# Kernel optimization log

Measured on AMD Instinct MI355X. Metric: run time of the kernel, lower is better.

## Reference

```python
import jax, jax.numpy as jnp
import numpy as np

B, T, H, D = 4, 4096, 16, 64
BLOCK_SIZE = 64      # BS: local block size
NUM_GLOBAL = 64      # G: global tokens (first G positions)
NUM_RANDOM = 192     # R: random key positions shared by all blocks


def setup_inputs() -> dict:
    key = jax.random.key(0)
    kq, kk, kv, kr = jax.random.split(key, 4)
    q = jax.random.normal(kq, (B, T, H, D), dtype=jnp.float32)
    k = jax.random.normal(kk, (B, T, H, D), dtype=jnp.float32)
    v = jax.random.normal(kv, (B, T, H, D), dtype=jnp.float32)
    # torch.randperm(src_len)[:R] -> no duplicate indices
    rand_idx = jax.random.permutation(kr, T)[:NUM_RANDOM].astype(jnp.int32)
    return {"q": q, "k": k, "v": v, "rand_idx": rand_idx}


def _bigbird(q, k, v, rand_idx):
    Bq, Tq, Hq, Dq = q.shape
    inv_scale = Dq ** (-0.5)
    G, BS, R = NUM_GLOBAL, BLOCK_SIZE, NUM_RANDOM

    # --- global queries: full attention over all keys ---
    gs = jnp.einsum('bghd,bkhd->bhgk', q[:, :G], k) * inv_scale
    gw = jax.nn.softmax(gs, axis=-1)
    out_g = jnp.einsum('bhgk,bkhd->bghd', gw, v)  # (B, G, H, D)

    # --- non-global queries: local block + global + random keys, one softmax ---
    nb = (Tq - G) // BS  # (T - G) divisible by BS by construction
    qb = q[:, G:].reshape(Bq, nb, BS, Hq, Dq)
    kb = k[:, G:].reshape(Bq, nb, BS, Hq, Dq)
    vb = v[:, G:].reshape(Bq, nb, BS, Hq, Dq)
    kg, vg = k[:, :G], v[:, :G]            # (B, G, H, D)
    kr, vr = k[:, rand_idx], v[:, rand_idx]  # (B, R, H, D)

    s_loc = jnp.einsum('bnlhd,bnkhd->bnhlk', qb, kb)   # (B, nb, H, BS, BS)
    s_glo = jnp.einsum('bnlhd,bkhd->bnhlk', qb, kg)    # (B, nb, H, BS, G)
    s_rnd = jnp.einsum('bnlhd,bkhd->bnhlk', qb, kr)    # (B, nb, H, BS, R)
    s = jnp.concatenate([s_loc, s_glo, s_rnd], axis=-1) * inv_scale
    w = jax.nn.softmax(s, axis=-1)  # joint softmax over local|global|random keys
    w_loc, w_glo, w_rnd = w[..., :BS], w[..., BS:BS + G], w[..., BS + G:]

    out_b = (jnp.einsum('bnhlk,bnkhd->bnlhd', w_loc, vb)
             + jnp.einsum('bnhlk,bkhd->bnlhd', w_glo, vg)
             + jnp.einsum('bnhlk,bkhd->bnlhd', w_rnd, vr))
    out_b = out_b.reshape(Bq, Tq - G, Hq, Dq)

    return jnp.concatenate([out_g, out_b], axis=1)  # (B, T, H, D)


def reference(q, k, v, rand_idx):
    return _bigbird(q, k, v, rand_idx)
```

## Files before the change

kernel.cpp:

```cpp
#include <hip/hip_runtime.h>
#include <math.h>
#include <stdint.h>

#define BB 4
#define TT 4096
#define HH 16
#define DD 64
#define GG 64
#define NRND 192
#define HD 1024
#define NBH 64
#define NCHUNK 4
#define NGBLK (NBH*NCHUNK)
#define NSPB  (NBH*63)

#define OFF_KBF  0ull
#define OFF_VT   33554432ull
#define OFF_KRT  67108864ull
#define OFF_VRT  68681728ull
#define OFF_WACC 70254592ull
#define OFF_WM   74448896ull
#define OFF_WL   74514432ull

typedef __attribute__((ext_vector_type(8))) short short8;
typedef __attribute__((ext_vector_type(16))) float f32x16;

__device__ __forceinline__ ushort rne_u(float f) {
    uint32_t u = __builtin_bit_cast(uint32_t, f);
    u += 0x7fffu + ((u >> 16) & 1u);
    return (ushort)(u >> 16);
}
__device__ __forceinline__ short bf_trunc_s(float f) {
    uint32_t u = __builtin_bit_cast(uint32_t, f);
    return (short)(u >> 16);
}
__device__ __forceinline__ float bf_back(short s) {
    uint32_t u = ((uint32_t)(uint16_t)s) << 16;
    return __builtin_bit_cast(float, u);
}
__device__ __forceinline__ short8 ld8u(const ushort* p) {
    typedef __attribute__((ext_vector_type(4))) short short4v;
    short4v a = *(const short4v*)p;
    short4v b = *(const short4v*)(p + 4);
    short8 r;
    r[0]=a[0]; r[1]=a[1]; r[2]=a[2]; r[3]=a[3];
    r[4]=b[0]; r[5]=b[1]; r[6]=b[2]; r[7]=b[3];
    return r;
}

typedef const __attribute__((address_space(1))) uint32_t* gas1_t;
typedef __attribute__((address_space(3))) uint32_t* las3_t;
__device__ __forceinline__ void gld16(const void* g, void* l) {
    __builtin_amdgcn_global_load_lds((gas1_t)g, (las3_t)l, 16, 0, 0);
}

__global__ __launch_bounds__(256, 4)
void bb_prep(const float* __restrict__ K, const float* __restrict__ V,
             const int* __restrict__ RIDX, char* __restrict__ ws)
{
    __shared__ ushort tl[64][68];
    __shared__ int toks[NRND];
    const int bid = blockIdx.x, tid = threadIdx.x;
    const int r  = tid >> 2;
    const int d0 = (tid & 3) * 16;

    if (bid < 8192) {
        const bool isK = bid < 4096;
        const int id = isK ? bid : bid - 4096;
        const int bh = id >> 6, tile = id & 63;
        const int b = bh >> 4, h = bh & 15;
        const float* src = (isK ? K : V) + ((size_t)b*TT*HH + h)*DD
                         + (size_t)(tile*64 + r)*HD + d0;
        float f[16];
        #pragma unroll
        for (int i = 0; i < 16; i += 4) {
            const float4 v4 = *(const float4*)(src + i);
            f[i]=v4.x; f[i+1]=v4.y; f[i+2]=v4.z; f[i+3]=v4.w;
        }
        if (isK) {
            #pragma unroll
            for (int i = 0; i < 16; ++i) tl[r][d0+i] = rne_u(f[i]);
        } else {
            #pragma unroll
            for (int i = 0; i < 16; ++i) tl[d0+i][r] = rne_u(f[i]);
        }
        __syncthreads();
        char* obase = ws + (isK ? OFF_KBF : OFF_VT)
                    + (size_t)bh*524288 + (size_t)tile*8192;
        #pragma unroll
        for (int e = 0; e < 2; ++e) {
            const int uu = tid*2 + e;
            const int c = uu >> 6, rr = uu & 63;
            *(short8*)(obase + c*1024 + rr*16) = ld8u(&tl[rr][c*8]);
        }
    } else {
        const int bh = bid - 8192;
        const int b = bh >> 4, h = bh & 15;
        const size_t base = ((size_t)b*TT*HH + h)*DD;
        if (tid < NRND) toks[tid] = RIDX[tid];
        __syncthreads();
        for (int sub = 0; sub < 3; ++sub) {
            const int tok = toks[sub*64 + r];
            float f[16];
            const float* ks = K + base + (size_t)tok*HD + d0;
            #pragma unroll
            for (int i = 0; i < 16; i += 4) {
                const float4 v4 = *(const float4*)(ks + i);
                f[i]=v4.x; f[i+1]=v4.y; f[i+2]=v4.z; f[i+3]=v4.w;
            }
            #pragma unroll
            for (int i = 0; i < 16; ++i) tl[r][d0+i] = rne_u(f[i]);
            __syncthreads();
            {
                char* obase = ws + OFF_KRT + (size_t)bh*24576 + (size_t)sub*8192;
                #pragma unroll
                for (int e = 0; e < 2; ++e) {
                    const int uu = tid*2 + e;
                    const int c = uu >> 6, rr = uu & 63;
                    *(short8*)(obase + c*1024 + rr*16) = ld8u(&tl[rr][c*8]);
                }
            }
            __syncthreads();
            const float* vs = V + base + (size_t)tok*HD + d0;
            #pragma unroll
            for (int i = 0; i < 16; i += 4) {
                const float4 v4 = *(const float4*)(vs + i);
                f[i]=v4.x; f[i+1]=v4.y; f[i+2]=v4.z; f[i+3]=v4.w;
            }
            #pragma unroll
            for (int i = 0; i < 16; ++i) tl[d0+i][r] = rne_u(f[i]);
            __syncthreads();
            {
                char* obase = ws + OFF_VRT + (size_t)bh*24576 + (size_t)sub*8192;
                #pragma unroll
                for (int e = 0; e < 2; ++e) {
                    const int uu = tid*2 + e;
                    const int c = uu >> 6, rr = uu & 63;
                    *(short8*)(obase + c*1024 + rr*16) = ld8u(&tl[rr][c*8]);
                }
            }
            __syncthreads();
        }
    }
}

__global__ __launch_bounds__(256, 4)
void bb_mfma(const float* __restrict__ Q, float* __restrict__ OUT,
             char* __restrict__ ws)
{
    __shared__ __align__(16) char smem[32768];
    __shared__ float sm_m[2][64];
    __shared__ float sm_l[2][64];
    float (*osum)[67] = (float(*)[67])smem;

    const int tid  = threadIdx.x;
    const int lane = tid & 63;
    const int wid  = tid >> 6;
    const int wq   = wid >> 1;
    const int wk   = wid & 1;
    const int lq   = lane & 31;
    const int lh   = lane >> 5;

    const int j = blockIdx.x;
    const bool is_glob = j < NGBLK;
    int bh, qtok0, ntiles, kt0 = 0, chunk = 0;
    if (is_glob) {
        chunk = j >> 6;
        bh    = (j & 7) + 8 * ((j >> 3) & 7);
        kt0   = chunk * 16;
        qtok0 = 0; ntiles = 16;
    } else {
        const int js = j - NGBLK;
        bh    = (js & 7) + 8 * ((js >> 3) & 7);
        qtok0 = GG + (js >> 6) * 64;
        ntiles = 5;
    }
    const int b  = bh >> 4;
    const int hd = bh & 15;
    const size_t bh_off = ((size_t)b * TT * HH + hd) * DD;

    const char* kbf_bh = ws + OFF_KBF + (size_t)bh * 524288;
    const char* vt_bh  = ws + OFF_VT  + (size_t)bh * 524288;
    const char* krt_bh = ws + OFF_KRT + (size_t)bh * 24576;
    const char* vrt_bh = ws + OFF_VRT + (size_t)bh * 24576;

    auto kbase = [&](int kt) -> const char* {
        if (is_glob)     return kbf_bh + (size_t)(kt0 + kt) * 8192;
        if (kt == 0)     return kbf_bh + (size_t)(qtok0 >> 6) * 8192;
        if (kt == 1)     return kbf_bh;
        return krt_bh + (size_t)(kt - 2) * 8192;
    };
    auto vbase = [&](int kt) -> const char* {
        if (is_glob)     return vt_bh + (size_t)(kt0 + kt) * 8192;
        if (kt == 0)     return vt_bh + (size_t)(qtok0 >> 6) * 8192;
        if (kt == 1)     return vt_bh;
        return vrt_bh + (size_t)(kt - 2) * 8192;
    };

    float4 qa[4], qb[4];
    {
        const float* qp = Q + bh_off + (size_t)(qtok0 + wq*32 + lq) * HD;
        #pragma unroll
        for (int ks = 0; ks < 4; ++ks) {
            qa[ks] = *(const float4*)(qp + ks*16 + lh*8);
            qb[ks] = *(const float4*)(qp + ks*16 + lh*8 + 4);
        }
    }

    auto stage = [&](int buf, int kt_t) {
        const char* kb = kbase(kt_t);
        const char* vb = vbase(kt_t);
        #pragma unroll
        for (int i = 0; i < 2; ++i) {
            const int c = wid*2 + i;
            gld16(kb + c*1024 + lane*16, smem + buf*8192 + c*1024);
            gld16(vb + c*1024 + lane*16, smem + 16384 + buf*8192 + c*1024);
        }
    };
    stage(0, 0);

    const float QSC = 0.18033688f;
    short8 qfh[4], qfl[4];
    #pragma unroll
    for (int ks = 0; ks < 4; ++ks) {
        float fv[8] = {qa[ks].x, qa[ks].y, qa[ks].z, qa[ks].w,
                       qb[ks].x, qb[ks].y, qb[ks].z, qb[ks].w};
        #pragma unroll
        for (int jj = 0; jj < 8; ++jj) {
            const float x = fv[jj] * QSC;
            const short hi = bf_trunc_s(x);
            qfh[ks][jj] = hi;
            qfl[ks][jj] = bf_trunc_s(x - bf_back(hi));
        }
    }

    f32x16 acc0, acc1;
    #pragma unroll
    for (int r = 0; r < 16; ++r) { acc0[r] = 0.f; acc1[r] = 0.f; }
    float m_run = -INFINITY, l_run = 0.f;

    for (int kt = 0; kt < ntiles; ++kt) {
        const int cur = kt & 1;
        const bool hn = (kt + 1 < ntiles);
        if (hn) {
            stage(cur ^ 1, kt + 1);
            asm volatile("s_waitcnt vmcnt(4)" ::: "memory");
        } else {
            asm volatile("s_waitcnt vmcnt(0)" ::: "memory");
        }
        __builtin_amdgcn_s_barrier();
        asm volatile("" ::: "memory");

        const char* kb = smem + cur*8192;
        const char* vb = smem + 16384 + cur*8192;

        f32x16 sc;
        #pragma unroll
        for (int r = 0; r < 16; ++r) sc[r] = 0.f;
        {
            const int krow = wk*32 + lq;
            #pragma unroll
            for (int ks = 0; ks < 4; ++ks) {
                const short8 ak = *(const short8*)(kb + (ks*2 + lh)*1024 + krow*16);
                sc = __builtin_amdgcn_mfma_f32_32x32x16_bf16(ak, qfh[ks], sc, 0, 0, 0);
                sc = __builtin_amdgcn_mfma_f32_32x32x16_bf16(ak, qfl[ks], sc, 0, 0, 0);
            }
        }

        float pm = sc[0];
        #pragma unroll
        for (int r = 1; r < 16; ++r) pm = fmaxf(pm, sc[r]);
        pm = fmaxf(pm, __shfl_xor(pm, 32));
        if (__any(pm > m_run + 11.5f)) {
            const float mnew = fmaxf(m_run, pm);
            const float cf = __builtin_exp2f(m_run - mnew);
            l_run *= cf;
            #pragma unroll
            for (int r = 0; r < 16; ++r) { acc0[r] *= cf; acc1[r] *= cf; }
            m_run = mnew;
        }
        float ls = 0.f;
        #pragma unroll
        for (int r = 0; r < 16; ++r) {
            sc[r] = __builtin_exp2f(sc[r] - m_run);
            ls += sc[r];
        }
        ls += __shfl_xor(ls, 32);
        l_run += ls;

        #pragma unroll
        for (int s = 0; s < 2; ++s) {
            uint32_t a01, a23, a45, a67;
            asm("v_cvt_pk_bf16_f32 %0, %1, %2" : "=v"(a01) : "v"(sc[8*s+0]), "v"(sc[8*s+1]));
            asm("v_cvt_pk_bf16_f32 %0, %1, %2" : "=v"(a23) : "v"(sc[8*s+2]), "v"(sc[8*s+3]));
            asm("v_cvt_pk_bf16_f32 %0, %1, %2" : "=v"(a45) : "v"(sc[8*s+4]), "v"(sc[8*s+5]));
            asm("v_cvt_pk_bf16_f32 %0, %1, %2" : "=v"(a67) : "v"(sc[8*s+6]), "v"(sc[8*s+7]));
            asm("v_permlane32_swap_b32 %0, %1" : "+v"(a01), "+v"(a45));
            asm("v_permlane32_swap_b32 %0, %1" : "+v"(a23), "+v"(a67));
            union { uint32_t u[4]; short8 v; } pfu;
            pfu.u[0] = a01; pfu.u[1] = a23; pfu.u[2] = a45; pfu.u[3] = a67;
            const int cb = wk*4 + s*2 + lh;
            const short8 v0 = *(const short8*)(vb + cb*1024 + lq*16);
            const short8 v1 = *(const short8*)(vb + cb*1024 + (lq + 32)*16);
            acc0 = __builtin_amdgcn_mfma_f32_32x32x16_bf16(v0, pfu.v, acc0, 0, 0, 0);
            acc1 = __builtin_amdgcn_mfma_f32_32x32x16_bf16(v1, pfu.v, acc1, 0, 0, 0);
        }

        if (hn) {
            asm volatile("" ::: "memory");
            __builtin_amdgcn_s_barrier();
            asm volatile("" ::: "memory");
        }
    }

    if (lane < 32) { sm_m[wk][wq*32 + lq] = m_run; sm_l[wk][wq*32 + lq] = l_run; }
    __syncthreads();
    const int qrow = wq*32 + lq;
    const float Mq  = fmaxf(sm_m[0][qrow], sm_m[1][qrow]);
    const float wsc = __builtin_exp2f(m_run - Mq);
    if (wk == 0) {
        #pragma unroll
        for (int r = 0; r < 16; ++r) {
            const int dr = (r & 3) + 8*(r >> 2) + 4*lh;
            osum[qrow][dr     ] = acc0[r] * wsc;
            osum[qrow][dr + 32] = acc1[r] * wsc;
        }
    }
    __syncthreads();
    if (wk == 1) {
        #pragma unroll
        for (int r = 0; r < 16; ++r) {
            const int dr = (r & 3) + 8*(r >> 2) + 4*lh;
            osum[qrow][dr     ] += acc0[r] * wsc;
            osum[qrow][dr + 32] += acc1[r] * wsc;
        }
    }
    __syncthreads();
    {
        const int q  = tid >> 2;
        const int d0 = (tid & 3) * 16;
        const float M     = fmaxf(sm_m[0][q], sm_m[1][q]);
        const float lcomb = __builtin_exp2f(sm_m[0][q] - M) * sm_l[0][q]
                          + __builtin_exp2f(sm_m[1][q] - M) * sm_l[1][q];
        if (is_glob) {
            float* WACC = (float*)(ws + OFF_WACC);
            float* WM   = (float*)(ws + OFF_WM);
            float* WL   = (float*)(ws + OFF_WL);
            const int slot = chunk * NBH + bh;
            float* dst = WACC + (size_t)slot * 4096 + q * 64 + d0;
            #pragma unroll
            for (int i = 0; i < 16; i += 4) {
                float4 o;
                o.x = osum[q][d0 + i    ];
                o.y = osum[q][d0 + i + 1];
                o.z = osum[q][d0 + i + 2];
                o.w = osum[q][d0 + i + 3];
                *(float4*)(dst + i) = o;
            }
            if ((tid & 3) == 0) {
                WM[slot * 64 + q] = M;
                WL[slot * 64 + q] = lcomb;
            }
        } else {
            const float inv = 1.f / lcomb;
            float* dst = OUT + bh_off + (size_t)(qtok0 + q) * HD + d0;
            #pragma unroll
            for (int i = 0; i < 16; i += 4) {
                float4 o;
                o.x = osum[q][d0 + i    ] * inv;
                o.y = osum[q][d0 + i + 1] * inv;
                o.z = osum[q][d0 + i + 2] * inv;
                o.w = osum[q][d0 + i + 3] * inv;
                *(float4*)(dst + i) = o;
            }
        }
    }
}

__global__ __launch_bounds__(256, 4)
void bb_combine(const char* __restrict__ ws, float* __restrict__ OUT)
{
    const int bh = blockIdx.x;
    const int b  = bh >> 4;
    const int hd = bh & 15;
    const size_t bh_off = ((size_t)b * TT * HH + hd) * DD;

    const float* WACC = (const float*)(ws + OFF_WACC);
    const float* WM   = (const float*)(ws + OFF_WM);
    const float* WL   = (const float*)(ws + OFF_WL);

    const int q  = threadIdx.x >> 2;
    const int d0 = (threadIdx.x & 3) * 16;

    float m[NCHUNK];
    float M = -INFINITY;
    #pragma unroll
    for (int c = 0; c < NCHUNK; ++c) {
        m[c] = WM[(c * NBH + bh) * 64 + q];
        M = fmaxf(M, m[c]);
    }
    float w[NCHUNK];
    float denom = 0.f;
    #pragma unroll
    for (int c = 0; c < NCHUNK; ++c) {
        w[c] = __builtin_exp2f(m[c] - M);
        denom += w[c] * WL[(c * NBH + bh) * 64 + q];
    }
    const float inv = 1.f / denom;

    float* dst = OUT + bh_off + (size_t)q * HD + d0;
    #pragma unroll
    for (int i = 0; i < 16; i += 4) {
        float ox = 0.f, oy = 0.f, oz = 0.f, ow = 0.f;
        #pragma unroll
        for (int c = 0; c < NCHUNK; ++c) {
            const float4 a = *(const float4*)&WACC[(size_t)(c * NBH + bh) * 4096 + q * 64 + d0 + i];
            ox += w[c] * a.x; oy += w[c] * a.y;
            oz += w[c] * a.z; ow += w[c] * a.w;
        }
        float4 o; o.x = ox * inv; o.y = oy * inv; o.z = oz * inv; o.w = ow * inv;
        *(float4*)(dst + i) = o;
    }
}

extern "C" void kernel_launch(void* const* d_in, const int* in_sizes, int n_in,
                              void* d_out, int out_size, void* d_ws, size_t ws_size,
                              hipStream_t stream) {
    const float* Q    = (const float*)d_in[0];
    const float* K    = (const float*)d_in[1];
    const float* V    = (const float*)d_in[2];
    const int*   RIDX = (const int*)d_in[3];
    float* OUT = (float*)d_out;
    char*  ws  = (char*)d_ws;

    hipLaunchKernelGGL(bb_prep, dim3(8192 + 64), dim3(256), 0, stream,
                       K, V, RIDX, ws);
    hipLaunchKernelGGL(bb_mfma, dim3(NGBLK + NSPB), dim3(256), 0, stream,
                       Q, OUT, ws);
    hipLaunchKernelGGL(bb_combine, dim3(NBH), dim3(256), 0, stream, ws, OUT);
}
```

Measured before the change: 123.1 us.

## Process 128-query blocks per workgroup to share global/random K/V tiles

Result: slower. 132.3 us (+7.5%).

```diff
diff --git a/kernel.cpp b/kernel.cpp
--- a/kernel.cpp
+++ b/kernel.cpp
@@ -10,9 +10,10 @@
 #define NRND 192
 #define HD 1024
 #define NBH 64
+#define QBLK 128
+#define NSPQ 32
 #define NCHUNK 4
-#define NGBLK (NBH*NCHUNK)
-#define NSPB  (NBH*63)
+#define SUBS (NCHUNK + NSPQ)
 
 #define OFF_KBF  0ull
 #define OFF_VT   33554432ull
@@ -37,6 +38,13 @@
 __device__ __forceinline__ float bf_back(short s) {
     uint32_t u = ((uint32_t)(uint16_t)s) << 16;
     return __builtin_bit_cast(float, u);
+}
+__device__ __forceinline__ float exp2_fast(float x) {
+#if __has_builtin(__builtin_amdgcn_exp2f)
+    return __builtin_amdgcn_exp2f(x);
+#else
+    float r; asm("v_exp_f32 %0, %1" : "=v"(r) : "v"(x)); return r;
+#endif
 }
 __device__ __forceinline__ short8 ld8u(const ushort* p) {
     typedef __attribute__((ext_vector_type(4))) short short4v;
@@ -144,13 +152,13 @@
     }
 }
 
-__global__ __launch_bounds__(256, 4)
+__global__ __launch_bounds__(512, 4)
 void bb_mfma(const float* __restrict__ Q, float* __restrict__ OUT,
              char* __restrict__ ws)
 {
-    __shared__ __align__(16) char smem[32768];
-    __shared__ float sm_m[2][64];
-    __shared__ float sm_l[2][64];
+    __shared__ __align__(16) char smem[34816];
+    __shared__ float sm_m[2][QBLK];
+    __shared__ float sm_l[2][QBLK];
     float (*osum)[67] = (float(*)[67])smem;
 
     const int tid  = threadIdx.x;
@@ -162,18 +170,19 @@
     const int lh   = lane >> 5;
 
     const int j = blockIdx.x;
-    const bool is_glob = j < NGBLK;
-    int bh, qtok0, ntiles, kt0 = 0, chunk = 0;
+    const int r = j & 63;
+    const int bh = ((r & 7) << 3) | (r >> 3);
+    const int sub = j >> 6;
+    const bool is_glob = sub < NCHUNK;
+    int qtok0, ntiles, kt0 = 0, chunk = 0, tA = 0, tB = 0;
     if (is_glob) {
-        chunk = j >> 6;
-        bh    = (j & 7) + 8 * ((j >> 3) & 7);
-        kt0   = chunk * 16;
-        qtok0 = 0; ntiles = 16;
+        chunk = sub; kt0 = chunk * 16; qtok0 = 0; ntiles = 16;
     } else {
-        const int js = j - NGBLK;
-        bh    = (js & 7) + 8 * ((js >> 3) & 7);
-        qtok0 = GG + (js >> 6) * 64;
-        ntiles = 5;
+        const int qi = sub - NCHUNK;
+        qtok0 = GG + qi * QBLK;
+        tA = 1 + 2 * qi;
+        tB = (qi == 31) ? 63 : 2 + 2 * qi;
+        ntiles = 6;
     }
     const int b  = bh >> 4;
     const int hd = bh & 15;
@@ -185,21 +194,27 @@
     const char* vrt_bh = ws + OFF_VRT + (size_t)bh * 24576;
 
     auto kbase = [&](int kt) -> const char* {
-        if (is_glob)     return kbf_bh + (size_t)(kt0 + kt) * 8192;
-        if (kt == 0)     return kbf_bh + (size_t)(qtok0 >> 6) * 8192;
-        if (kt == 1)     return kbf_bh;
-        return krt_bh + (size_t)(kt - 2) * 8192;
+        if (is_glob) return kbf_bh + (size_t)(kt0 + kt) * 8192;
+        if (kt == 0) return kbf_bh + (size_t)tA * 8192;
+        if (kt == 1) return kbf_bh + (size_t)tB * 8192;
+        if (kt == 2) return kbf_bh;
+        return krt_bh + (size_t)(kt - 3) * 8192;
     };
     auto vbase = [&](int kt) -> const char* {
-        if (is_glob)     return vt_bh + (size_t)(kt0 + kt) * 8192;
-        if (kt == 0)     return vt_bh + (size_t)(qtok0 >> 6) * 8192;
-        if (kt == 1)     return vt_bh;
-        return vrt_bh + (size_t)(kt - 2) * 8192;
+        if (is_glob) return vt_bh + (size_t)(kt0 + kt) * 8192;
+        if (kt == 0) return vt_bh + (size_t)tA * 8192;
+        if (kt == 1) return vt_bh + (size_t)tB * 8192;
+        if (kt == 2) return vt_bh;
+        return vrt_bh + (size_t)(kt - 3) * 8192;
     };
 
+    const int qrow = wq * 32 + lq;
+    int qoff;
+    if (is_glob) qoff = qrow & 63;
+    else         qoff = (qtok0 + qrow < TT) ? qrow : (qrow & 63);
     float4 qa[4], qb[4];
     {
-        const float* qp = Q + bh_off + (size_t)(qtok0 + wq*32 + lq) * HD;
+        const float* qp = Q + bh_off + (size_t)(qtok0 + qoff) * HD;
         #pragma unroll
         for (int ks = 0; ks < 4; ++ks) {
             qa[ks] = *(const float4*)(qp + ks*16 + lh*8);
@@ -207,15 +222,13 @@
         }
     }
 
+    char* kbuf = smem;
+    char* vbuf = smem + 16384;
     auto stage = [&](int buf, int kt_t) {
         const char* kb = kbase(kt_t);
         const char* vb = vbase(kt_t);
-        #pragma unroll
-        for (int i = 0; i < 2; ++i) {
-            const int c = wid*2 + i;
-            gld16(kb + c*1024 + lane*16, smem + buf*8192 + c*1024);
-            gld16(vb + c*1024 + lane*16, smem + 16384 + buf*8192 + c*1024);
-        }
+        gld16(kb + wid*1024 + lane*16, kbuf + buf*8192 + wid*1024);
+        gld16(vb + wid*1024 + lane*16, vbuf + buf*8192 + wid*1024);
     };
     stage(0, 0);
 
@@ -236,7 +249,7 @@
 
     f32x16 acc0, acc1;
     #pragma unroll
-    for (int r = 0; r < 16; ++r) { acc0[r] = 0.f; acc1[r] = 0.f; }
+    for (int rr = 0; rr < 16; ++rr) { acc0[rr] = 0.f; acc1[rr] = 0.f; }
     float m_run = -INFINITY, l_run = 0.f;
 
     for (int kt = 0; kt < ntiles; ++kt) {
@@ -244,66 +257,75 @@
         const bool hn = (kt + 1 < ntiles);
         if (hn) {
             stage(cur ^ 1, kt + 1);
-            asm volatile("s_waitcnt vmcnt(4)" ::: "memory");
+            asm volatile("s_waitcnt vmcnt(2)" ::: "memory");
         } else {
             asm volatile("s_waitcnt vmcnt(0)" ::: "memory");
         }
         __builtin_amdgcn_s_barrier();
         asm volatile("" ::: "memory");
 
-        const char* kb = smem + cur*8192;
-        const char* vb = smem + 16384 + cur*8192;
-
-        f32x16 sc;
-        #pragma unroll
-        for (int r = 0; r < 16; ++r) sc[r] = 0.f;
-        {
-            const int krow = wk*32 + lq;
-            #pragma unroll
-            for (int ks = 0; ks < 4; ++ks) {
-                const short8 ak = *(const short8*)(kb + (ks*2 + lh)*1024 + krow*16);
-                sc = __builtin_amdgcn_mfma_f32_32x32x16_bf16(ak, qfh[ks], sc, 0, 0, 0);
-                sc = __builtin_amdgcn_mfma_f32_32x32x16_bf16(ak, qfl[ks], sc, 0, 0, 0);
-            }
-        }
-
-        float pm = sc[0];
-        #pragma unroll
-        for (int r = 1; r < 16; ++r) pm = fmaxf(pm, sc[r]);
-        pm = fmaxf(pm, __shfl_xor(pm, 32));
-        if (__any(pm > m_run + 11.5f)) {
-            const float mnew = fmaxf(m_run, pm);
-            const float cf = __builtin_exp2f(m_run - mnew);
-            l_run *= cf;
-            #pragma unroll
-            for (int r = 0; r < 16; ++r) { acc0[r] *= cf; acc1[r] *= cf; }
-            m_run = mnew;
-        }
-        float ls = 0.f;
-        #pragma unroll
-        for (int r = 0; r < 16; ++r) {
-            sc[r] = __builtin_exp2f(sc[r] - m_run);
-            ls += sc[r];
-        }
-        ls += __shfl_xor(ls, 32);
-        l_run += ls;
-
-        #pragma unroll
-        for (int s = 0; s < 2; ++s) {
-            uint32_t a01, a23, a45, a67;
-            asm("v_cvt_pk_bf16_f32 %0, %1, %2" : "=v"(a01) : "v"(sc[8*s+0]), "v"(sc[8*s+1]));
-            asm("v_cvt_pk_bf16_f32 %0, %1, %2" : "=v"(a23) : "v"(sc[8*s+2]), "v"(sc[8*s+3]));
-            asm("v_cvt_pk_bf16_f32 %0, %1, %2" : "=v"(a45) : "v"(sc[8*s+4]), "v"(sc[8*s+5]));
-            asm("v_cvt_pk_bf16_f32 %0, %1, %2" : "=v"(a67) : "v"(sc[8*s+6]), "v"(sc[8*s+7]));
-            asm("v_permlane32_swap_b32 %0, %1" : "+v"(a01), "+v"(a45));
-            asm("v_permlane32_swap_b32 %0, %1" : "+v"(a23), "+v"(a67));
-            union { uint32_t u[4]; short8 v; } pfu;
-            pfu.u[0] = a01; pfu.u[1] = a23; pfu.u[2] = a45; pfu.u[3] = a67;
-            const int cb = wk*4 + s*2 + lh;
-            const short8 v0 = *(const short8*)(vb + cb*1024 + lq*16);
-            const short8 v1 = *(const short8*)(vb + cb*1024 + (lq + 32)*16);
-            acc0 = __builtin_amdgcn_mfma_f32_32x32x16_bf16(v0, pfu.v, acc0, 0, 0, 0);
-            acc1 = __builtin_amdgcn_mfma_f32_32x32x16_bf16(v1, pfu.v, acc1, 0, 0, 0);
+        const bool act = is_glob ? true
+                       : (kt == 0) ? (wq < 2)
+                       : (kt == 1) ? (wq >= 2) : true;
+        if (act) {
+            const char* kb = kbuf + cur*8192;
+            const char* vb = vbuf + cur*8192;
+
+            f32x16 sc;
+            #pragma unroll
+            for (int rr = 0; rr < 16; ++rr) sc[rr] = 0.f;
+            {
+                const int krow = wk*32 + lq;
+                __builtin_amdgcn_s_setprio(1);
+                #pragma unroll
+                for (int ks = 0; ks < 4; ++ks) {
+                    const short8 ak = *(const short8*)(kb + (ks*2 + lh)*1024 + krow*16);
+                    sc = __builtin_amdgcn_mfma_f32_32x32x16_bf16(ak, qfh[ks], sc, 0, 0, 0);
+                    sc = __builtin_amdgcn_mfma_f32_32x32x16_bf16(ak, qfl[ks], sc, 0, 0, 0);
+                }
+                __builtin_amdgcn_s_setprio(0);
+            }
+
+            float pm = sc[0];
+            #pragma unroll
+            for (int rr = 1; rr < 16; ++rr) pm = fmaxf(pm, sc[rr]);
+            pm = fmaxf(pm, __shfl_xor(pm, 32));
+            if (__any(pm > m_run + 11.5f)) {
+                const float mnew = fmaxf(m_run, pm);
+                const float cf = exp2_fast(m_run - mnew);
+                l_run *= cf;
+                #pragma unroll
+                for (int rr = 0; rr < 16; ++rr) { acc0[rr] *= cf; acc1[rr] *= cf; }
+                m_run = mnew;
+            }
+            float ls = 0.f;
+            #pragma unroll
+            for (int rr = 0; rr < 16; ++rr) {
+                sc[rr] = exp2_fast(sc[rr] - m_run);
+                ls += sc[rr];
+            }
+            ls += __shfl_xor(ls, 32);
+            l_run += ls;
+
+            #pragma unroll
+            for (int s = 0; s < 2; ++s) {
+                uint32_t a01, a23, a45, a67;
+                asm("v_cvt_pk_bf16_f32 %0, %1, %2" : "=v"(a01) : "v"(sc[8*s+0]), "v"(sc[8*s+1]));
+                asm("v_cvt_pk_bf16_f32 %0, %1, %2" : "=v"(a23) : "v"(sc[8*s+2]), "v"(sc[8*s+3]));
+                asm("v_cvt_pk_bf16_f32 %0, %1, %2" : "=v"(a45) : "v"(sc[8*s+4]), "v"(sc[8*s+5]));
+                asm("v_cvt_pk_bf16_f32 %0, %1, %2" : "=v"(a67) : "v"(sc[8*s+6]), "v"(sc[8*s+7]));
+                asm("v_permlane32_swap_b32 %0, %1" : "+v"(a01), "+v"(a45));
+                asm("v_permlane32_swap_b32 %0, %1" : "+v"(a23), "+v"(a67));
+                union { uint32_t u[4]; short8 v; } pfu;
+                pfu.u[0] = a01; pfu.u[1] = a23; pfu.u[2] = a45; pfu.u[3] = a67;
+                const int cb = wk*4 + s*2 + lh;
+                const short8 v0 = *(const short8*)(vb + cb*1024 + lq*16);
+                const short8 v1 = *(const short8*)(vb + cb*1024 + (lq + 32)*16);
+                __builtin_amdgcn_s_setprio(1);
+                acc0 = __builtin_amdgcn_mfma_f32_32x32x16_bf16(v0, pfu.v, acc0, 0, 0, 0);
+                acc1 = __builtin_amdgcn_mfma_f32_32x32x16_bf16(v1, pfu.v, acc1, 0, 0, 0);
+                __builtin_amdgcn_s_setprio(0);
+            }
         }
 
         if (hn) {
@@ -313,26 +335,25 @@
         }
     }
 
-    if (lane < 32) { sm_m[wk][wq*32 + lq] = m_run; sm_l[wk][wq*32 + lq] = l_run; }
+    if (lane < 32) { sm_m[wk][qrow] = m_run; sm_l[wk][qrow] = l_run; }
     __syncthreads();
-    const int qrow = wq*32 + lq;
     const float Mq  = fmaxf(sm_m[0][qrow], sm_m[1][qrow]);
-    const float wsc = __builtin_exp2f(m_run - Mq);
+    const float wsc = exp2_fast(m_run - Mq);
     if (wk == 0) {
         #pragma unroll
-        for (int r = 0; r < 16; ++r) {
-            const int dr = (r & 3) + 8*(r >> 2) + 4*lh;
-            osum[qrow][dr     ] = acc0[r] * wsc;
-            osum[qrow][dr + 32] = acc1[r] * wsc;
+        for (int rr = 0; rr < 16; ++rr) {
+            const int dr = (rr & 3) + 8*(rr >> 2) + 4*lh;
+            osum[qrow][dr     ] = acc0[rr] * wsc;
+            osum[qrow][dr + 32] = acc1[rr] * wsc;
         }
     }
     __syncthreads();
     if (wk == 1) {
         #pragma unroll
-        for (int r = 0; r < 16; ++r) {
-            const int dr = (r & 3) + 8*(r >> 2) + 4*lh;
-            osum[qrow][dr     ] += acc0[r] * wsc;
-            osum[qrow][dr + 32] += acc1[r] * wsc;
+        for (int rr = 0; rr < 16; ++rr) {
+            const int dr = (rr & 3) + 8*(rr >> 2) + 4*lh;
+            osum[qrow][dr     ] += acc0[rr] * wsc;
+            osum[qrow][dr + 32] += acc1[rr] * wsc;
         }
     }
     __syncthreads();
@@ -340,28 +361,30 @@
         const int q  = tid >> 2;
         const int d0 = (tid & 3) * 16;
         const float M     = fmaxf(sm_m[0][q], sm_m[1][q]);
-        const float lcomb = __builtin_exp2f(sm_m[0][q] - M) * sm_l[0][q]
-                          + __builtin_exp2f(sm_m[1][q] - M) * sm_l[1][q];
+        const float lcomb = exp2_fast(sm_m[0][q] - M) * sm_l[0][q]
+                          + exp2_fast(sm_m[1][q] - M) * sm_l[1][q];
         if (is_glob) {
-            float* WACC = (float*)(ws + OFF_WACC);
-            float* WM   = (float*)(ws + OFF_WM);
-            float* WL   = (float*)(ws + OFF_WL);
-            const int slot = chunk * NBH + bh;
-            float* dst = WACC + (size_t)slot * 4096 + q * 64 + d0;
-            #pragma unroll
-            for (int i = 0; i < 16; i += 4) {
-                float4 o;
-                o.x = osum[q][d0 + i    ];
-                o.y = osum[q][d0 + i + 1];
-                o.z = osum[q][d0 + i + 2];
-                o.w = osum[q][d0 + i + 3];
-                *(float4*)(dst + i) = o;
-            }
-            if ((tid & 3) == 0) {
-                WM[slot * 64 + q] = M;
-                WL[slot * 64 + q] = lcomb;
-            }
-        } else {
+            if (q < 64) {
+                float* WACC = (float*)(ws + OFF_WACC);
+                float* WM   = (float*)(ws + OFF_WM);
+                float* WL   = (float*)(ws + OFF_WL);
+                const int slot = chunk * NBH + bh;
+                float* dst = WACC + (size_t)slot * 4096 + q * 64 + d0;
+                #pragma unroll
+                for (int i = 0; i < 16; i += 4) {
+                    float4 o;
+                    o.x = osum[q][d0 + i    ];
+                    o.y = osum[q][d0 + i + 1];
+                    o.z = osum[q][d0 + i + 2];
+                    o.w = osum[q][d0 + i + 3];
+                    *(float4*)(dst + i) = o;
+                }
+                if ((tid & 3) == 0) {
+                    WM[slot * 64 + q] = M;
+                    WL[slot * 64 + q] = lcomb;
+                }
+            }
+        } else if (qtok0 + q < TT) {
             const float inv = 1.f / lcomb;
             float* dst = OUT + bh_off + (size_t)(qtok0 + q) * HD + d0;
             #pragma unroll
@@ -403,7 +426,7 @@
     float denom = 0.f;
     #pragma unroll
     for (int c = 0; c < NCHUNK; ++c) {
-        w[c] = __builtin_exp2f(m[c] - M);
+        w[c] = exp2_fast(m[c] - M);
         denom += w[c] * WL[(c * NBH + bh) * 64 + q];
     }
     const float inv = 1.f / denom;
@@ -435,7 +458,7 @@
 
     hipLaunchKernelGGL(bb_prep, dim3(8192 + 64), dim3(256), 0, stream,
                        K, V, RIDX, ws);
-    hipLaunchKernelGGL(bb_mfma, dim3(NGBLK + NSPB), dim3(256), 0, stream,
+    hipLaunchKernelGGL(bb_mfma, dim3(NBH * SUBS), dim3(512), 0, stream,
                        Q, OUT, ws);
     hipLaunchKernelGGL(bb_combine, dim3(NBH), dim3(256), 0, stream, ws, OUT);
 }
```
